# Kernel tuning notes

Measured on AMD Instinct MI355X. Metric: run time of the kernel, lower is better.

Reference implementation:

```python
import jax, jax.numpy as jnp
import numpy as np

B, S, M, D, H = 16, 128, 128, 256, 256  # batch, src nodes, max neighbors, emb dim, hidden dim


def setup_inputs() -> dict:
    key = jax.random.key(0)
    k1, k2, k3, k4 = jax.random.split(key, 4)
    src = jax.random.normal(k1, (B, S, M, D), dtype=jnp.float32)
    neigh = jax.random.normal(k2, (B, S, M, D), dtype=jnp.float32)
    # ragged neighbor lists: zero out rows past each node's neighbor count,
    # matching the torch module's all-zero-row padding convention
    lens = jax.random.randint(k3, (B, S), 1, M + 1)
    valid = (jnp.arange(M)[None, None, :] < lens[:, :, None]).astype(jnp.float32)
    neigh = neigh * valid[..., None]
    W_map = jax.random.normal(k4, (2 * D, H), dtype=jnp.float32) * np.float32(1.0 / np.sqrt(2 * D))
    b_map = jnp.zeros((H,), dtype=jnp.float32)
    return {"src_node_features": src, "neigh_node_features": neigh, "W_map": W_map, "b_map": b_map}


def reference(src_node_features, neigh_node_features, W_map, b_map):
    # NeighborAggregator, method='mean': count non-all-zero neighbor rows, masked mean
    valid = jnp.any(neigh_node_features != 0, axis=-1)            # [B, S, M]
    num = jnp.sum(valid, axis=-1).astype(src_node_features.dtype)  # [B, S]
    neigh_mean = neigh_node_features.sum(axis=2) / jnp.maximum(num, 1.0)[..., None]  # [B, S, D]
    # SynGCNLayer, agg_hidden_method='concat'
    hidden = jnp.concatenate([src_node_features.sum(axis=2), neigh_mean], axis=-1)  # [B, S, 2D]
    # filter_nonsource_nodes: all src slots populated -> identity reshape to [B*S, 2D]
    hidden = hidden.reshape(-1, hidden.shape[-1])
    out = jax.nn.leaky_relu(hidden @ W_map + b_map, negative_slope=0.01)  # [B*S, H]
    # normalize=False, dropout is identity in eval
    return out
```

## Files before the change

### kernel.cpp

```cpp
#include <hip/hip_runtime.h>

#define Bdim 16
#define Sdim 128
#define Mdim 128
#define Ddim 256
#define Hdim 256
#define NPB 2
#define NT  512

__global__ __launch_bounds__(NT, 4) void gcn_fused4(
    const float* __restrict__ src,
    const float* __restrict__ neigh,
    const float* __restrict__ Wmap,
    const float* __restrict__ bmap,
    float* __restrict__ out)
{
    const int tid   = threadIdx.x;
    const int wave  = tid >> 6;
    const int lane  = tid & 63;
    const int lnode = wave >> 2;
    const int mph   = wave & 3;

    const size_t base4 = (size_t)(blockIdx.x * NPB + lnode) * (Mdim * Ddim / 4);
    const float4* __restrict__ src4 = (const float4*)src + base4 + (size_t)(mph * 32) * (Ddim / 4) + lane;
    const float4* __restrict__ ngh4 = (const float4*)neigh + base4 + (size_t)(mph * 32) * (Ddim / 4) + lane;

    float4 sacc = make_float4(0.f, 0.f, 0.f, 0.f);
    float4 nacc = make_float4(0.f, 0.f, 0.f, 0.f);
    int cnt = 0;

    for (int i0 = 0; i0 < 32; i0 += 8) {
        float4 sv[8], nv[8];
        #pragma unroll
        for (int j = 0; j < 8; ++j) {
            const int idx = (i0 + j) * (Ddim / 4);
            sv[j] = src4[idx];
            nv[j] = ngh4[idx];
        }
        #pragma unroll
        for (int j = 0; j < 8; ++j) {
            sacc.x += sv[j].x; sacc.y += sv[j].y; sacc.z += sv[j].z; sacc.w += sv[j].w;
            nacc.x += nv[j].x; nacc.y += nv[j].y; nacc.z += nv[j].z; nacc.w += nv[j].w;
            int nz = (nv[j].x != 0.f) | (nv[j].y != 0.f) | (nv[j].z != 0.f) | (nv[j].w != 0.f);
            if (__any(nz)) cnt++;
        }
    }

    __shared__ float s_s[8][Ddim];
    __shared__ float s_n[8][Ddim];
    __shared__ int   s_cnt[8];
    __shared__ float hid[NPB][2 * Ddim];

    *(float4*)&s_s[wave][lane * 4] = sacc;
    *(float4*)&s_n[wave][lane * 4] = nacc;
    if (lane == 0) s_cnt[wave] = cnt;
    __syncthreads();

    {
        const int t    = tid & (Ddim - 1);
        const int half = tid >> 8;
        #pragma unroll
        for (int n = 0; n < NPB; ++n) {
            if (half == 0) {
                hid[n][t] = (s_s[4 * n][t] + s_s[4 * n + 1][t])
                          + (s_s[4 * n + 2][t] + s_s[4 * n + 3][t]);
            } else {
                const float num = (float)(s_cnt[4 * n] + s_cnt[4 * n + 1]
                                        + s_cnt[4 * n + 2] + s_cnt[4 * n + 3]);
                const float inv = 1.0f / fmaxf(num, 1.0f);
                hid[n][Ddim + t] = ((s_n[4 * n][t] + s_n[4 * n + 1][t])
                                  + (s_n[4 * n + 2][t] + s_n[4 * n + 3][t])) * inv;
            }
        }
    }
    __syncthreads();

    const int t = tid & (Ddim - 1);
    const int n = tid >> 8;
    float acc0 = bmap[t];
    float acc1 = 0.f;
    const float4* __restrict__ h = (const float4*)hid[n];

    #pragma unroll 4
    for (int k4 = 0; k4 < (2 * Ddim) / 4; ++k4) {
        const float4 ha = h[k4];
        const int k = k4 * 4;
        const float w0 = Wmap[(size_t)(k + 0) * Hdim + t];
        const float w1 = Wmap[(size_t)(k + 1) * Hdim + t];
        const float w2 = Wmap[(size_t)(k + 2) * Hdim + t];
        const float w3 = Wmap[(size_t)(k + 3) * Hdim + t];
        acc0 = fmaf(ha.x, w0, acc0);
        acc1 = fmaf(ha.y, w1, acc1);
        acc0 = fmaf(ha.z, w2, acc0);
        acc1 = fmaf(ha.w, w3, acc1);
    }

    const float acc = acc0 + acc1;
    const float r = acc > 0.f ? acc : 0.01f * acc;
    out[(size_t)(blockIdx.x * NPB + n) * Hdim + t] = r;
}

extern "C" void kernel_launch(void* const* d_in, const int* in_sizes, int n_in,
                              void* d_out, int out_size, void* d_ws, size_t ws_size,
                              hipStream_t stream) {
    const float* src   = (const float*)d_in[0];
    const float* neigh = (const float*)d_in[1];
    const float* Wmap  = (const float*)d_in[2];
    const float* bmap  = (const float*)d_in[3];
    float* out = (float*)d_out;

    dim3 grid((Bdim * Sdim) / NPB);
    dim3 block(NT);
    gcn_fused4<<<grid, block, 0, stream>>>(src, neigh, Wmap, bmap, out);
}
```

Before: 519.0 us.

## Stream neighbor/source rows into LDS via global_load_lds double buffering

Replaces the direct register float4 loads of the src and neigh rows with asynchronous global-to-LDS DMA (global_load_lds, 16 bytes per lane), double-buffered per wave with manual vmcnt waits, then reads the data back from LDS to accumulate. The staging LDS is reused for the partial-sum reduction. The aim is to keep more memory traffic in flight with fewer VGPRs on this bandwidth-bound reduction. In exchange it uses 64KB+ of LDS per block, which cuts occupancy below the launch-bounds target. The prefetch depth is also only one chunk of two rows, and it adds an extra LDS round trip.

```diff
diff --git a/kernel.cpp b/kernel.cpp
--- a/kernel.cpp
+++ b/kernel.cpp
@@ -8,7 +8,7 @@
 #define NPB 2
 #define NT  512
 
-__global__ __launch_bounds__(NT, 4) void gcn_fused4(
+__global__ __launch_bounds__(NT, 4) void gcn_dma(
     const float* __restrict__ src,
     const float* __restrict__ neigh,
     const float* __restrict__ Wmap,
@@ -21,38 +21,59 @@
     const int lnode = wave >> 2;
     const int mph   = wave & 3;
 
-    const size_t base4 = (size_t)(blockIdx.x * NPB + lnode) * (Mdim * Ddim / 4);
-    const float4* __restrict__ src4 = (const float4*)src + base4 + (size_t)(mph * 32) * (Ddim / 4) + lane;
-    const float4* __restrict__ ngh4 = (const float4*)neigh + base4 + (size_t)(mph * 32) * (Ddim / 4) + lane;
+    __shared__ __align__(16) float lds[8 * 2048];
+    __shared__ float hid[NPB][2 * Ddim];
+    __shared__ int   s_cnt[8];
+
+    float* stg = &lds[wave * 2048];
+
+    const size_t node = (size_t)(blockIdx.x * NPB + lnode);
+    const size_t rowbase = node * (Mdim * Ddim) + (size_t)(mph * 32) * Ddim;
+    const float* gs = src   + rowbase + lane * 4;
+    const float* gn = neigh + rowbase + lane * 4;
+
+    #define DMA16(gp, lp)                                                     \
+        __builtin_amdgcn_global_load_lds(                                     \
+            (const __attribute__((address_space(1))) void*)(gp),              \
+            (__attribute__((address_space(3))) void*)(lp), 16, 0, 0)
+
+    #define ISSUE(c)                                                          \
+        do {                                                                  \
+            const int _b = ((c) & 1) * 512;                                   \
+            DMA16(gs + ((c) * 2 + 0) * Ddim, stg + _b);                       \
+            DMA16(gs + ((c) * 2 + 1) * Ddim, stg + _b + 256);                 \
+            DMA16(gn + ((c) * 2 + 0) * Ddim, stg + 1024 + _b);                \
+            DMA16(gn + ((c) * 2 + 1) * Ddim, stg + 1024 + _b + 256);          \
+        } while (0)
 
     float4 sacc = make_float4(0.f, 0.f, 0.f, 0.f);
     float4 nacc = make_float4(0.f, 0.f, 0.f, 0.f);
     int cnt = 0;
 
-    for (int i0 = 0; i0 < 32; i0 += 8) {
-        float4 sv[8], nv[8];
+    ISSUE(0);
+    for (int c = 0; c < 16; ++c) {
+        if (c < 15) {
+            ISSUE(c + 1);
+            asm volatile("s_waitcnt vmcnt(4)" ::: "memory");
+        } else {
+            asm volatile("s_waitcnt vmcnt(0)" ::: "memory");
+        }
+        const int b = (c & 1) * 512;
         #pragma unroll
-        for (int j = 0; j < 8; ++j) {
-            const int idx = (i0 + j) * (Ddim / 4);
-            sv[j] = src4[idx];
-            nv[j] = ngh4[idx];
-        }
-        #pragma unroll
-        for (int j = 0; j < 8; ++j) {
-            sacc.x += sv[j].x; sacc.y += sv[j].y; sacc.z += sv[j].z; sacc.w += sv[j].w;
-            nacc.x += nv[j].x; nacc.y += nv[j].y; nacc.z += nv[j].z; nacc.w += nv[j].w;
-            int nz = (nv[j].x != 0.f) | (nv[j].y != 0.f) | (nv[j].z != 0.f) | (nv[j].w != 0.f);
+        for (int r = 0; r < 2; ++r) {
+            const float4 sv = *(const float4*)&stg[b + r * 256 + lane * 4];
+            const float4 nv = *(const float4*)&stg[1024 + b + r * 256 + lane * 4];
+            sacc.x += sv.x; sacc.y += sv.y; sacc.z += sv.z; sacc.w += sv.w;
+            nacc.x += nv.x; nacc.y += nv.y; nacc.z += nv.z; nacc.w += nv.w;
+            int nz = (nv.x != 0.f) | (nv.y != 0.f) | (nv.z != 0.f) | (nv.w != 0.f);
             if (__any(nz)) cnt++;
         }
     }
+    #undef ISSUE
+    #undef DMA16
 
-    __shared__ float s_s[8][Ddim];
-    __shared__ float s_n[8][Ddim];
-    __shared__ int   s_cnt[8];
-    __shared__ float hid[NPB][2 * Ddim];
-
-    *(float4*)&s_s[wave][lane * 4] = sacc;
-    *(float4*)&s_n[wave][lane * 4] = nacc;
+    *(float4*)&stg[lane * 4]       = sacc;
+    *(float4*)&stg[256 + lane * 4] = nacc;
     if (lane == 0) s_cnt[wave] = cnt;
     __syncthreads();
 
@@ -62,14 +83,15 @@
         #pragma unroll
         for (int n = 0; n < NPB; ++n) {
             if (half == 0) {
-                hid[n][t] = (s_s[4 * n][t] + s_s[4 * n + 1][t])
-                          + (s_s[4 * n + 2][t] + s_s[4 * n + 3][t]);
+                hid[n][t] = (lds[(4 * n + 0) * 2048 + t] + lds[(4 * n + 1) * 2048 + t])
+                          + (lds[(4 * n + 2) * 2048 + t] + lds[(4 * n + 3) * 2048 + t]);
             } else {
                 const float num = (float)(s_cnt[4 * n] + s_cnt[4 * n + 1]
                                         + s_cnt[4 * n + 2] + s_cnt[4 * n + 3]);
                 const float inv = 1.0f / fmaxf(num, 1.0f);
-                hid[n][Ddim + t] = ((s_n[4 * n][t] + s_n[4 * n + 1][t])
-                                  + (s_n[4 * n + 2][t] + s_n[4 * n + 3][t])) * inv;
+                hid[n][Ddim + t] =
+                    ((lds[(4 * n + 0) * 2048 + 256 + t] + lds[(4 * n + 1) * 2048 + 256 + t])
+                   + (lds[(4 * n + 2) * 2048 + 256 + t] + lds[(4 * n + 3) * 2048 + 256 + t])) * inv;
             }
         }
     }
@@ -111,5 +133,5 @@
 
     dim3 grid((Bdim * Sdim) / NPB);
     dim3 block(NT);
-    gcn_fused4<<<grid, block, 0, stream>>>(src, neigh, Wmap, bmap, out);
+    gcn_dma<<<grid, block, 0, stream>>>(src, neigh, Wmap, bmap, out);
 }
```

Result: no change. 524.8 us (+1.1%).
